# Kernel tuning notes

Measured on AMD Instinct MI355X. Metric: run time of the kernel, lower is better.

The kernel has to match this reference:

```python
import jax, jax.numpy as jnp
import numpy as np

B, N, Mdim, CS, INP, OUT = 256, 2048, 64, 512, 256, 256
ADDR_R = Mdim + 6          # k(M), beta(1), g(1), s(3), gamma(1)
ADDR_W = 3 * Mdim + 6      # + erase(M) + add(M)


def setup_inputs() -> dict:
    key = jax.random.key(0)
    ks = jax.random.split(key, 16)
    s = 0.05
    x = jax.random.normal(ks[0], (B, INP), dtype=jnp.float32)
    memory = jax.random.uniform(ks[1], (B, N, Mdim), dtype=jnp.float32) * 0.1 + 1e-6
    h = jax.random.normal(ks[2], (B, CS), dtype=jnp.float32) * 0.1
    c = jax.random.normal(ks[3], (B, CS), dtype=jnp.float32) * 0.1
    rw = jax.random.uniform(ks[4], (B, N), dtype=jnp.float32)
    read_w = rw / rw.sum(axis=1, keepdims=True)
    ww = jax.random.uniform(ks[5], (B, N), dtype=jnp.float32)
    write_w = ww / ww.sum(axis=1, keepdims=True)
    prev_read = jax.random.normal(ks[6], (B, Mdim), dtype=jnp.float32) * 0.1
    W_ih = jax.random.normal(ks[7], (4 * CS, INP + Mdim), dtype=jnp.float32) * s
    W_hh = jax.random.normal(ks[8], (4 * CS, CS), dtype=jnp.float32) * s
    b_ih = jnp.zeros((4 * CS,), jnp.float32)
    b_hh = jnp.zeros((4 * CS,), jnp.float32)
    W_r = jax.random.normal(ks[9], (ADDR_R, CS), dtype=jnp.float32) * s
    b_r = jnp.zeros((ADDR_R,), jnp.float32)
    W_w = jax.random.normal(ks[10], (ADDR_W, CS), dtype=jnp.float32) * s
    b_w = jnp.zeros((ADDR_W,), jnp.float32)
    W_o = jax.random.normal(ks[11], (OUT, CS + Mdim), dtype=jnp.float32) * s
    b_o = jnp.zeros((OUT,), jnp.float32)
    return dict(x=x, memory=memory, h=h, c=c, read_w=read_w, write_w=write_w,
                prev_read=prev_read, W_ih=W_ih, W_hh=W_hh, b_ih=b_ih, b_hh=b_hh,
                W_r=W_r, b_r=b_r, W_w=W_w, b_w=b_w, W_o=W_o, b_o=b_o)


def _addressing(out_vec, prev_w, memory, M):
    # Eq. 5-9: content softmax, interpolation, circular shift, sharpening.
    k = out_vec[:, :M]                                   # [B, M]
    beta = jax.nn.softplus(out_vec[:, M:M + 1])          # [B, 1]
    g = jax.nn.sigmoid(out_vec[:, M + 1:M + 2])          # [B, 1]
    s = jax.nn.softmax(out_vec[:, M + 2:M + 5], axis=1)  # [B, 3]
    gamma = 1.0 + jax.nn.softplus(out_vec[:, M + 5:M + 6])
    norm_k = jnp.linalg.norm(k, axis=1, keepdims=True) + 1e-8        # [B, 1]
    norm_mem = jnp.linalg.norm(memory, axis=2) + 1e-8                # [B, N]
    sim = jnp.einsum('bnm,bm->bn', memory, k) / (norm_k * norm_mem)  # cosine
    w_c = jax.nn.softmax(beta * sim, axis=1)
    w_g = g * w_c + (1.0 - g) * prev_w
    # circular convolution with 3-tap shift kernel (replaces the roll loop)
    w_s = (s[:, 0:1] * jnp.roll(w_g, 1, axis=1)
           + s[:, 1:2] * w_g
           + s[:, 2:3] * jnp.roll(w_g, -1, axis=1))
    w_pow = w_s ** gamma
    return w_pow / (w_pow.sum(axis=1, keepdims=True) + 1e-8)


def reference(x, memory, h, c, read_w, write_w, prev_read,
              W_ih, W_hh, b_ih, b_hh, W_r, b_r, W_w, b_w, W_o, b_o):
    M = memory.shape[2]
    inp = jnp.concatenate([x, prev_read], axis=1)
    gates = inp @ W_ih.T + b_ih + h @ W_hh.T + b_hh
    i_g, f_g, g_g, o_g = jnp.split(gates, 4, axis=1)  # torch LSTMCell gate order
    i_g = jax.nn.sigmoid(i_g); f_g = jax.nn.sigmoid(f_g)
    g_g = jnp.tanh(g_g); o_g = jax.nn.sigmoid(o_g)
    c_new = f_g * c + i_g * g_g
    h_new = o_g * jnp.tanh(c_new)
    # read head (uses pre-write memory)
    read_out = h_new @ W_r.T + b_r
    w_read = _addressing(read_out, read_w, memory, M)
    read_vec = jnp.einsum('bn,bnm->bm', w_read, memory)
    # write head: address, then erase/add outer-product update
    write_out = h_new @ W_w.T + b_w
    w_write = _addressing(write_out, write_w, memory, M)
    erase = jax.nn.sigmoid(write_out[:, M + 6:2 * M + 6])
    add = write_out[:, 2 * M + 6:3 * M + 6]
    memory_new = memory * (1.0 - w_write[:, :, None] * erase[:, None, :]) \
                 + w_write[:, :, None] * add[:, None, :]
    out = jnp.concatenate([h_new, read_vec], axis=1) @ W_o.T + b_o
    return (out, memory_new, h_new, c_new, w_read, w_write, read_vec)
```

## Files before the change

kernel.cpp:

```cpp
#include <hip/hip_runtime.h>
#include <math.h>

#define Bsz   256
#define Nn    2048
#define Md    64
#define CSd   512
#define INPd  256
#define OUTd  256
#define KTOT  832
#define PSTRIDE 272
#define GSZ   524288
#define ZSPL  8
#define KZ    104

__device__ __forceinline__ float sigmoidf_(float x){ return 1.f/(1.f+expf(-x)); }
__device__ __forceinline__ float softplusf_(float x){ return fmaxf(x,0.f) + log1pf(expf(-fabsf(x))); }

__device__ __forceinline__ float4 loadA4(const float* __restrict__ x, const float* __restrict__ pr,
                                         const float* __restrict__ h, int row, int k){
  if (k < INPd)            return *(const float4*)&x[row*INPd + k];
  else if (k < INPd+Md)    return *(const float4*)&pr[row*Md + (k-INPd)];
  else                     return *(const float4*)&h[row*CSd + (k-INPd-Md)];
}
__device__ __forceinline__ float4 loadW4(const float* __restrict__ Wih, const float* __restrict__ Whh,
                                         int j, int k){
  if (k < INPd+Md)         return *(const float4*)&Wih[j*(INPd+Md) + k];
  else                     return *(const float4*)&Whh[j*CSd + (k-INPd-Md)];
}

__global__ __launch_bounds__(64) void k_gates(
    const float* __restrict__ x, const float* __restrict__ prev_read, const float* __restrict__ h,
    const float* __restrict__ W_ih, const float* __restrict__ W_hh,
    float* __restrict__ partials)
{
  __shared__ __align__(16) float As[8][68];
  __shared__ __align__(16) float Bs[8][68];
  const int t = threadIdx.x;
  const int col0 = blockIdx.x * 64;
  const int row0 = blockIdx.y * 64;
  const int z    = blockIdx.z;
  const int tr = t >> 3, tc = t & 7;
  const int row = row0 + t;
  const int j   = col0 + t;

  float acc[8][8] = {};
  float4 a0, a1, b0, b1;
  int kb = z * KZ;
  a0 = loadA4(x, prev_read, h, row, kb);   a1 = loadA4(x, prev_read, h, row, kb+4);
  b0 = loadW4(W_ih, W_hh, j, kb);          b1 = loadW4(W_ih, W_hh, j, kb+4);

  for (int kc = 0; kc < 13; ++kc) {
    As[0][t]=a0.x; As[1][t]=a0.y; As[2][t]=a0.z; As[3][t]=a0.w;
    As[4][t]=a1.x; As[5][t]=a1.y; As[6][t]=a1.z; As[7][t]=a1.w;
    Bs[0][t]=b0.x; Bs[1][t]=b0.y; Bs[2][t]=b0.z; Bs[3][t]=b0.w;
    Bs[4][t]=b1.x; Bs[5][t]=b1.y; Bs[6][t]=b1.z; Bs[7][t]=b1.w;
    __syncthreads();
    if (kc < 12) {
      int kn = kb + (kc+1)*8;
      a0 = loadA4(x, prev_read, h, row, kn);   a1 = loadA4(x, prev_read, h, row, kn+4);
      b0 = loadW4(W_ih, W_hh, j, kn);          b1 = loadW4(W_ih, W_hh, j, kn+4);
    }
    #pragma unroll
    for (int kk = 0; kk < 8; ++kk) {
      float av[8], bv[8];
      *(float4*)&av[0] = *(const float4*)&As[kk][tr*8];
      *(float4*)&av[4] = *(const float4*)&As[kk][tr*8+4];
      *(float4*)&bv[0] = *(const float4*)&Bs[kk][tc*8];
      *(float4*)&bv[4] = *(const float4*)&Bs[kk][tc*8+4];
      #pragma unroll
      for (int i=0;i<8;++i)
        #pragma unroll
        for (int q=0;q<8;++q)
          acc[i][q] += av[i]*bv[q];
    }
    __syncthreads();
  }
  float* part = partials + (size_t)z * GSZ;
  #pragma unroll
  for (int i=0;i<8;++i) {
    int r = row0 + tr*8 + i;
    float4 v0 = {acc[i][0],acc[i][1],acc[i][2],acc[i][3]};
    float4 v1 = {acc[i][4],acc[i][5],acc[i][6],acc[i][7]};
    *(float4*)&part[r*2048 + col0 + tc*8]     = v0;
    *(float4*)&part[r*2048 + col0 + tc*8 + 4] = v1;
  }
}

__global__ __launch_bounds__(512) void k_lstm_heads(
    const float* __restrict__ partials, const float* __restrict__ c,
    const float* __restrict__ b_ih, const float* __restrict__ b_hh,
    const float* __restrict__ W_r, const float* __restrict__ b_r,
    const float* __restrict__ W_w, const float* __restrict__ b_w,
    float* __restrict__ h_new, float* __restrict__ c_new, float* __restrict__ params)
{
  __shared__ float hs[CSd];
  __shared__ float ob[268];
  int b = blockIdx.x, t = threadIdx.x;
  float g[4];
  #pragma unroll
  for (int q = 0; q < 4; ++q) {
    int col = q*512 + t;
    float s = b_ih[col] + b_hh[col];
    #pragma unroll
    for (int sp = 0; sp < ZSPL; ++sp) s += partials[(size_t)sp*GSZ + b*2048 + col];
    g[q] = s;
  }
  float ig = sigmoidf_(g[0]);
  float fg = sigmoidf_(g[1]);
  float gg = tanhf(g[2]);
  float og = sigmoidf_(g[3]);
  float cn = fg * c[b*CSd + t] + ig * gg;
  float hn = og * tanhf(cn);
  c_new[b*CSd + t] = cn;
  h_new[b*CSd + t] = hn;
  hs[t] = hn;
  __syncthreads();
  int wave = t >> 6, lane = t & 63;
  for (int r = wave; r < 268; r += 8) {
    const float* wrow; float bias;
    if (r < 70) { wrow = W_r + r*CSd;      bias = b_r[r]; }
    else        { wrow = W_w + (r-70)*CSd; bias = b_w[r-70]; }
    float s = 0.f;
    #pragma unroll
    for (int i = 0; i < 8; ++i) s += wrow[i*64 + lane] * hs[i*64 + lane];
    #pragma unroll
    for (int off = 32; off; off >>= 1) s += __shfl_xor(s, off);
    if (lane == 0) ob[r] = s + bias;
  }
  __syncthreads();
  float* P = params + b*PSTRIDE;
  if (t < 256) {
    if (t < 64)       P[t] = ob[t];
    else if (t < 128) P[t] = ob[70 + (t-64)];
    else if (t < 192) P[t] = sigmoidf_(ob[140 + (t-128)]);
    else              P[t] = ob[204 + (t-192)];
  }
  float* S = P + 256;
  if (wave == 0) {
    float v = ob[lane]; float sq = v*v;
    #pragma unroll
    for (int off = 32; off; off >>= 1) sq += __shfl_xor(sq, off);
    if (lane == 0) S[6] = 1.f/(sqrtf(sq)+1e-8f);
  } else if (wave == 1) {
    float v = ob[70 + lane]; float sq = v*v;
    #pragma unroll
    for (int off = 32; off; off >>= 1) sq += __shfl_xor(sq, off);
    if (lane == 0) S[13] = 1.f/(sqrtf(sq)+1e-8f);
  }
  if (t == 128) {
    S[0] = softplusf_(ob[64]);
    S[1] = sigmoidf_(ob[65]);
    float m3 = fmaxf(ob[66], fmaxf(ob[67], ob[68]));
    float e0=expf(ob[66]-m3), e1=expf(ob[67]-m3), e2=expf(ob[68]-m3);
    float es = e0+e1+e2;
    S[2]=e0/es; S[3]=e1/es; S[4]=e2/es;
    S[5] = 1.f + softplusf_(ob[69]);
  }
  if (t == 129) {
    S[7] = softplusf_(ob[134]);
    S[8] = sigmoidf_(ob[135]);
    float m3 = fmaxf(ob[136], fmaxf(ob[137], ob[138]));
    float e0=expf(ob[136]-m3), e1=expf(ob[137]-m3), e2=expf(ob[138]-m3);
    float es = e0+e1+e2;
    S[9]=e0/es; S[10]=e1/es; S[11]=e2/es;
    S[12] = 1.f + softplusf_(ob[139]);
  }
}

__global__ __launch_bounds__(256) void k_sim(
    const float* __restrict__ mem, const float* __restrict__ params,
    float* __restrict__ a_r, float* __restrict__ a_w)
{
  int b = blockIdx.y;
  int n = blockIdx.x*16 + (threadIdx.x >> 4);
  int chunk = threadIdx.x & 15;
  float4 v = ((const float4*)mem)[(b*Nn + n)*16 + chunk];
  const float* P = params + b*PSTRIDE;
  float4 kr = ((const float4*)P)[chunk];
  float4 kw = ((const float4*)(P+64))[chunk];
  float ss = v.x*v.x + v.y*v.y + v.z*v.z + v.w*v.w;
  float pr = v.x*kr.x + v.y*kr.y + v.z*kr.z + v.w*kr.w;
  float pw = v.x*kw.x + v.y*kw.y + v.z*kw.z + v.w*kw.w;
  #pragma unroll
  for (int off=8; off; off>>=1) {
    ss += __shfl_xor(ss, off);
    pr += __shfl_xor(pr, off);
    pw += __shfl_xor(pw, off);
  }
  if (chunk == 0) {
    float inv_nm = 1.f/(sqrtf(ss)+1e-8f);
    const float* S = P + 256;
    a_r[b*Nn+n] = S[0] * pr * S[6]  * inv_nm;
    a_w[b*Nn+n] = S[7] * pw * S[13] * inv_nm;
  }
}

__device__ __forceinline__ float block_reduce512(float val, float* red, int t, bool ismax){
  #pragma unroll
  for (int off=32; off; off>>=1)
    val = ismax ? fmaxf(val, __shfl_xor(val,off)) : val + __shfl_xor(val,off);
  __syncthreads();
  if ((t&63)==0) red[t>>6] = val;
  __syncthreads();
  float r = red[0];
  if (ismax) { for (int i=1;i<8;++i) r = fmaxf(r, red[i]); }
  else       { for (int i=1;i<8;++i) r += red[i]; }
  return r;
}

__global__ __launch_bounds__(512) void k_weights(
    const float* __restrict__ a_r, const float* __restrict__ a_w,
    const float* __restrict__ read_w, const float* __restrict__ write_w,
    const float* __restrict__ params,
    float* __restrict__ w_read, float* __restrict__ w_write)
{
  __shared__ float wg[Nn];
  __shared__ float red[8];
  int b = blockIdx.x;
  int which = blockIdx.y;
  const float* a    = which ? a_w     : a_r;
  const float* prev = which ? write_w : read_w;
  float* outw       = which ? w_write : w_read;
  const float* S = params + b*PSTRIDE + 256 + (which ? 7 : 0);
  float g = S[1], s0 = S[2], s1 = S[3], s2 = S[4], gamma = S[5];
  int t = threadIdx.x;
  float v[4];
  #pragma unroll
  for (int i=0;i<4;++i) v[i] = a[b*Nn + t*4+i];
  float lmax = fmaxf(fmaxf(v[0],v[1]), fmaxf(v[2],v[3]));
  float mx = block_reduce512(lmax, red, t, true);
  float e[4]; float ps = 0.f;
  #pragma unroll
  for (int i=0;i<4;++i){ e[i] = expf(v[i]-mx); ps += e[i]; }
  float denom = block_reduce512(ps, red, t, false);
  float inv = 1.f/denom;
  #pragma unroll
  for (int i=0;i<4;++i){
    float wc = e[i]*inv;
    wg[t*4+i] = g*wc + (1.f-g)*prev[b*Nn + t*4+i];
  }
  __syncthreads();
  float wp[4]; float psum = 0.f;
  #pragma unroll
  for (int i=0;i<4;++i){
    int n = t*4+i;
    float wsv = s0*wg[(n+Nn-1)&(Nn-1)] + s1*wg[n] + s2*wg[(n+1)&(Nn-1)];
    wp[i] = powf(wsv, gamma);
    psum += wp[i];
  }
  float tot = block_reduce512(psum, red, t, false);
  float invt = 1.f/(tot + 1e-8f);
  #pragma unroll
  for (int i=0;i<4;++i) outw[b*Nn + t*4+i] = wp[i]*invt;
}

__global__ __launch_bounds__(256) void k_memupd(
    const float* __restrict__ mem, const float* __restrict__ params,
    const float* __restrict__ w_read, const float* __restrict__ w_write,
    float* __restrict__ mem_new, float* __restrict__ prv)
{
  __shared__ __align__(16) float er[64];
  __shared__ __align__(16) float ad[64];
  __shared__ float4 part[64];
  int b = blockIdx.y;
  int n0 = blockIdx.x * 64;
  int t = threadIdx.x;
  const float* P = params + b*PSTRIDE;
  if (t < 64)       er[t]    = P[128+t];
  else if (t < 128) ad[t-64] = P[192+(t-64)];
  __syncthreads();
  int chunk = t & 15;
  int rr = t >> 4;
  float4 e4 = ((const float4*)er)[chunk];
  float4 a4 = ((const float4*)ad)[chunk];
  float4 acc = {0.f,0.f,0.f,0.f};
  #pragma unroll
  for (int p = 0; p < 4; ++p) {
    int n = n0 + p*16 + rr;
    float4 v = ((const float4*)mem)[(b*Nn+n)*16 + chunk];
    float ww = w_write[b*Nn+n];
    float wr = w_read[b*Nn+n];
    float4 o;
    o.x = v.x*(1.f-ww*e4.x) + ww*a4.x;
    o.y = v.y*(1.f-ww*e4.y) + ww*a4.y;
    o.z = v.z*(1.f-ww*e4.z) + ww*a4.z;
    o.w = v.w*(1.f-ww*e4.w) + ww*a4.w;
    ((float4*)mem_new)[(b*Nn+n)*16 + chunk] = o;
    acc.x += wr*v.x; acc.y += wr*v.y; acc.z += wr*v.z; acc.w += wr*v.w;
  }
  #pragma unroll
  for (int off = 16; off <= 32; off <<= 1) {
    acc.x += __shfl_xor(acc.x, off);
    acc.y += __shfl_xor(acc.y, off);
    acc.z += __shfl_xor(acc.z, off);
    acc.w += __shfl_xor(acc.w, off);
  }
  int wave = t >> 6;
  if ((t & 63) < 16) part[wave*16 + chunk] = acc;
  __syncthreads();
  if (t < 16) {
    float4 s = part[t];
    for (int w=1; w<4; ++w){ float4 q = part[w*16+t]; s.x+=q.x; s.y+=q.y; s.z+=q.z; s.w+=q.w; }
    *(float4*)&prv[(b*32 + blockIdx.x)*64 + t*4] = s;
  }
}

__global__ __launch_bounds__(256) void k_out(
    const float* __restrict__ h_new, const float* __restrict__ prv,
    const float* __restrict__ W_o, const float* __restrict__ b_o,
    float* __restrict__ out, float* __restrict__ read_vec)
{
  __shared__ float vbuf[576];
  int b = blockIdx.y, t = threadIdx.x;
  vbuf[t]     = h_new[b*CSd + t];
  vbuf[t+256] = h_new[b*CSd + t + 256];
  if (t < 64) {
    float s = 0.f;
    #pragma unroll 8
    for (int i = 0; i < 32; ++i) s += prv[(b*32 + i)*64 + t];
    vbuf[512+t] = s;
    if (blockIdx.x == 0) read_vec[b*64 + t] = s;
  }
  __syncthreads();
  int wave = t >> 6, lane = t & 63;
  float vb[9];
  #pragma unroll
  for (int i = 0; i < 9; ++i) vb[i] = vbuf[i*64 + lane];
  int cbase = blockIdx.x*64 + wave*16;
  for (int jj = 0; jj < 16; ++jj) {
    int cc = cbase + jj;
    const float* w = W_o + cc*576;
    float s = 0.f;
    #pragma unroll
    for (int i = 0; i < 9; ++i) s += w[i*64 + lane] * vb[i];
    #pragma unroll
    for (int off = 32; off; off >>= 1) s += __shfl_xor(s, off);
    if (lane == 0) out[b*OUTd + cc] = s + b_o[cc];
  }
}

extern "C" void kernel_launch(void* const* d_in, const int* in_sizes, int n_in,
                              void* d_out, int out_size, void* d_ws, size_t ws_size,
                              hipStream_t stream)
{
  const float* x         = (const float*)d_in[0];
  const float* memory    = (const float*)d_in[1];
  const float* h         = (const float*)d_in[2];
  const float* c         = (const float*)d_in[3];
  const float* read_w    = (const float*)d_in[4];
  const float* write_w   = (const float*)d_in[5];
  const float* prev_read = (const float*)d_in[6];
  const float* W_ih      = (const float*)d_in[7];
  const float* W_hh      = (const float*)d_in[8];
  const float* b_ih      = (const float*)d_in[9];
  const float* b_hh      = (const float*)d_in[10];
  const float* W_r       = (const float*)d_in[11];
  const float* b_r       = (const float*)d_in[12];
  const float* W_w       = (const float*)d_in[13];
  const float* b_w       = (const float*)d_in[14];
  const float* W_o       = (const float*)d_in[15];
  const float* b_o       = (const float*)d_in[16];

  float* out      = (float*)d_out;
  float* mem_new  = out + 256*256;
  float* h_new    = mem_new + (size_t)256*2048*64;
  float* c_new    = h_new + 256*512;
  float* w_read   = c_new + 256*512;
  float* w_write  = w_read + 256*2048;
  float* read_vec = w_write + 256*2048;

  float* ws       = (float*)d_ws;
  float* params   = ws;
  float* partials = params + 256*PSTRIDE;
  float* a_r      = partials;
  float* a_w      = partials + GSZ;
  float* prv      = partials + 2*GSZ;

  k_gates     <<<dim3(32,4,ZSPL), 64, 0, stream>>>(x, prev_read, h, W_ih, W_hh, partials);
  k_lstm_heads<<<256,            512, 0, stream>>>(partials, c, b_ih, b_hh, W_r, b_r, W_w, b_w,
                                                   h_new, c_new, params);
  k_sim       <<<dim3(128,256),  256, 0, stream>>>(memory, params, a_r, a_w);
  k_weights   <<<dim3(256,2),    512, 0, stream>>>(a_r, a_w, read_w, write_w, params, w_read, w_write);
  k_memupd    <<<dim3(32,256),   256, 0, stream>>>(memory, params, w_read, w_write, mem_new, prv);
  k_out       <<<dim3(4,256),    256, 0, stream>>>(h_new, prv, W_o, b_o, out, read_vec);
}
```

Baseline: 370.0 us.

## Retile gate GEMM to 256-thread blocks and coarsen similarity kernel rows

The gate GEMM now runs 256 threads per block, each computing a 4x4 micro-tile with a 16-wide K chunk. Split-K drops from 8 to 4 slices, which halves the partial-sum buffer traffic and gives more waves per block. The similarity kernel has each thread process four memory rows, so the grid is four times smaller and the key and scale loads are amortised. The trade-off is lower register reuse per thread in the GEMM and less K-parallelism, which risks lower arithmetic intensity per thread.

```diff
diff --git a/kernel.cpp b/kernel.cpp
--- a/kernel.cpp
+++ b/kernel.cpp
@@ -10,8 +10,8 @@
 #define KTOT  832
 #define PSTRIDE 272
 #define GSZ   524288
-#define ZSPL  8
-#define KZ    104
+#define ZSPL  4
+#define KZ    208
 
 __device__ __forceinline__ float sigmoidf_(float x){ return 1.f/(1.f+expf(-x)); }
 __device__ __forceinline__ float softplusf_(float x){ return fmaxf(x,0.f) + log1pf(expf(-fabsf(x))); }
@@ -28,61 +28,56 @@
   else                     return *(const float4*)&Whh[j*CSd + (k-INPd-Md)];
 }
 
-__global__ __launch_bounds__(64) void k_gates(
+__global__ __launch_bounds__(256) void k_gates(
     const float* __restrict__ x, const float* __restrict__ prev_read, const float* __restrict__ h,
     const float* __restrict__ W_ih, const float* __restrict__ W_hh,
     float* __restrict__ partials)
 {
-  __shared__ __align__(16) float As[8][68];
-  __shared__ __align__(16) float Bs[8][68];
+  __shared__ __align__(16) float As[16][68];
+  __shared__ __align__(16) float Bs[16][68];
   const int t = threadIdx.x;
   const int col0 = blockIdx.x * 64;
   const int row0 = blockIdx.y * 64;
   const int z    = blockIdx.z;
-  const int tr = t >> 3, tc = t & 7;
-  const int row = row0 + t;
-  const int j   = col0 + t;
-
-  float acc[8][8] = {};
-  float4 a0, a1, b0, b1;
+  const int lr = t >> 2;
+  const int kq = (t & 3) * 4;
+  const int tr = t >> 4, tc = t & 15;
+  const int arow = row0 + lr;
+  const int bcol = col0 + lr;
+
+  float acc[4][4] = {};
   int kb = z * KZ;
-  a0 = loadA4(x, prev_read, h, row, kb);   a1 = loadA4(x, prev_read, h, row, kb+4);
-  b0 = loadW4(W_ih, W_hh, j, kb);          b1 = loadW4(W_ih, W_hh, j, kb+4);
+  float4 a  = loadA4(x, prev_read, h, arow, kb + kq);
+  float4 bq = loadW4(W_ih, W_hh, bcol, kb + kq);
 
   for (int kc = 0; kc < 13; ++kc) {
-    As[0][t]=a0.x; As[1][t]=a0.y; As[2][t]=a0.z; As[3][t]=a0.w;
-    As[4][t]=a1.x; As[5][t]=a1.y; As[6][t]=a1.z; As[7][t]=a1.w;
-    Bs[0][t]=b0.x; Bs[1][t]=b0.y; Bs[2][t]=b0.z; Bs[3][t]=b0.w;
-    Bs[4][t]=b1.x; Bs[5][t]=b1.y; Bs[6][t]=b1.z; Bs[7][t]=b1.w;
+    As[kq+0][lr] = a.x;  As[kq+1][lr] = a.y;  As[kq+2][lr] = a.z;  As[kq+3][lr] = a.w;
+    Bs[kq+0][lr] = bq.x; Bs[kq+1][lr] = bq.y; Bs[kq+2][lr] = bq.z; Bs[kq+3][lr] = bq.w;
     __syncthreads();
     if (kc < 12) {
-      int kn = kb + (kc+1)*8;
-      a0 = loadA4(x, prev_read, h, row, kn);   a1 = loadA4(x, prev_read, h, row, kn+4);
-      b0 = loadW4(W_ih, W_hh, j, kn);          b1 = loadW4(W_ih, W_hh, j, kn+4);
+      int kn = kb + (kc+1)*16 + kq;
+      a  = loadA4(x, prev_read, h, arow, kn);
+      bq = loadW4(W_ih, W_hh, bcol, kn);
     }
     #pragma unroll
-    for (int kk = 0; kk < 8; ++kk) {
-      float av[8], bv[8];
-      *(float4*)&av[0] = *(const float4*)&As[kk][tr*8];
-      *(float4*)&av[4] = *(const float4*)&As[kk][tr*8+4];
-      *(float4*)&bv[0] = *(const float4*)&Bs[kk][tc*8];
-      *(float4*)&bv[4] = *(const float4*)&Bs[kk][tc*8+4];
+    for (int kk = 0; kk < 16; ++kk) {
+      float av[4], bv[4];
+      *(float4*)&av[0] = *(const float4*)&As[kk][tr*4];
+      *(float4*)&bv[0] = *(const float4*)&Bs[kk][tc*4];
       #pragma unroll
-      for (int i=0;i<8;++i)
+      for (int i=0;i<4;++i)
         #pragma unroll
-        for (int q=0;q<8;++q)
+        for (int q=0;q<4;++q)
           acc[i][q] += av[i]*bv[q];
     }
     __syncthreads();
   }
   float* part = partials + (size_t)z * GSZ;
   #pragma unroll
-  for (int i=0;i<8;++i) {
-    int r = row0 + tr*8 + i;
+  for (int i=0;i<4;++i) {
+    int r = row0 + tr*4 + i;
     float4 v0 = {acc[i][0],acc[i][1],acc[i][2],acc[i][3]};
-    float4 v1 = {acc[i][4],acc[i][5],acc[i][6],acc[i][7]};
-    *(float4*)&part[r*2048 + col0 + tc*8]     = v0;
-    *(float4*)&part[r*2048 + col0 + tc*8 + 4] = v1;
+    *(float4*)&part[r*2048 + col0 + tc*4] = v0;
   }
 }
 
@@ -172,26 +167,33 @@
     float* __restrict__ a_r, float* __restrict__ a_w)
 {
   int b = blockIdx.y;
-  int n = blockIdx.x*16 + (threadIdx.x >> 4);
+  int n0 = blockIdx.x * 64;
+  int rr = threadIdx.x >> 4;
   int chunk = threadIdx.x & 15;
-  float4 v = ((const float4*)mem)[(b*Nn + n)*16 + chunk];
   const float* P = params + b*PSTRIDE;
   float4 kr = ((const float4*)P)[chunk];
   float4 kw = ((const float4*)(P+64))[chunk];
-  float ss = v.x*v.x + v.y*v.y + v.z*v.z + v.w*v.w;
-  float pr = v.x*kr.x + v.y*kr.y + v.z*kr.z + v.w*kr.w;
-  float pw = v.x*kw.x + v.y*kw.y + v.z*kw.z + v.w*kw.w;
-  #pragma unroll
-  for (int off=8; off; off>>=1) {
-    ss += __shfl_xor(ss, off);
-    pr += __shfl_xor(pr, off);
-    pw += __shfl_xor(pw, off);
-  }
-  if (chunk == 0) {
-    float inv_nm = 1.f/(sqrtf(ss)+1e-8f);
-    const float* S = P + 256;
-    a_r[b*Nn+n] = S[0] * pr * S[6]  * inv_nm;
-    a_w[b*Nn+n] = S[7] * pw * S[13] * inv_nm;
+  const float* S = P + 256;
+  float cr = S[0] * S[6];
+  float cw = S[7] * S[13];
+  #pragma unroll
+  for (int p = 0; p < 4; ++p) {
+    int n = n0 + p*16 + rr;
+    float4 v = ((const float4*)mem)[(b*Nn + n)*16 + chunk];
+    float ss = v.x*v.x + v.y*v.y + v.z*v.z + v.w*v.w;
+    float pr = v.x*kr.x + v.y*kr.y + v.z*kr.z + v.w*kr.w;
+    float pw = v.x*kw.x + v.y*kw.y + v.z*kw.z + v.w*kw.w;
+    #pragma unroll
+    for (int off=8; off; off>>=1) {
+      ss += __shfl_xor(ss, off);
+      pr += __shfl_xor(pr, off);
+      pw += __shfl_xor(pw, off);
+    }
+    if (chunk == 0) {
+      float inv_nm = 1.f/(sqrtf(ss)+1e-8f);
+      a_r[b*Nn+n] = cr * pr * inv_nm;
+      a_w[b*Nn+n] = cw * pw * inv_nm;
+    }
   }
 }
 
@@ -376,10 +378,10 @@
   float* a_w      = partials + GSZ;
   float* prv      = partials + 2*GSZ;
 
-  k_gates     <<<dim3(32,4,ZSPL), 64, 0, stream>>>(x, prev_read, h, W_ih, W_hh, partials);
+  k_gates     <<<dim3(32,4,ZSPL), 256, 0, stream>>>(x, prev_read, h, W_ih, W_hh, partials);
   k_lstm_heads<<<256,            512, 0, stream>>>(partials, c, b_ih, b_hh, W_r, b_r, W_w, b_w,
                                                    h_new, c_new, params);
-  k_sim       <<<dim3(128,256),  256, 0, stream>>>(memory, params, a_r, a_w);
+  k_sim       <<<dim3(32,256),   256, 0, stream>>>(memory, params, a_r, a_w);
   k_weights   <<<dim3(256,2),    512, 0, stream>>>(a_r, a_w, read_w, write_w, params, w_read, w_write);
   k_memupd    <<<dim3(32,256),   256, 0, stream>>>(memory, params, w_read, w_write, mem_new, prv);
   k_out       <<<dim3(4,256),    256, 0, stream>>>(h_new, prv, W_o, b_o, out, read_vec);
```

After: 365.9 us. No clear change (-1.1%).
